# Kernel tuning notes

Hardware: AMD Instinct MI355X
Metric: run time of the kernel (lower is better)

## Reference

```python
import jax, jax.numpy as jnp
import numpy as np

E, D, A, EMB, V = 2048, 512, 512, 512, 10000
B, HW, L = 64, 14, 52
P = HW * HW  # num_pixels
T = L - 1    # max decode length (we force max caption length == L)


def setup_inputs() -> dict:
    key = jax.random.key(0)
    ks = jax.random.split(key, 24)
    s = 0.02
    inp = {
        "encoder_out": jax.random.normal(ks[0], (B, HW, HW, E), jnp.float32),
        "encoded_captions": jax.random.randint(ks[1], (B, L), 0, V),
        "caption_lengths": jax.random.randint(ks[2], (B, 1), 2, L + 1).at[0, 0].set(L),
        # attention
        "W_ea": jax.random.normal(ks[3], (A, E)) * s, "b_ea": jnp.zeros((A,)),
        "W_da": jax.random.normal(ks[4], (A, D)) * s, "b_da": jnp.zeros((A,)),
        "w_fa": jax.random.normal(ks[5], (1, A)) * s, "b_fa": jnp.zeros((1,)),
        # embedding (uniform(-0.1,0.1) as in init_weights)
        "emb_table": jax.random.uniform(ks[6], (V, EMB), minval=-0.1, maxval=0.1),
        # LSTMCell: gates order i,f,g,o
        "W_ih": jax.random.normal(ks[7], (4 * D, EMB + E)) * s, "b_ih": jnp.zeros((4 * D,)),
        "W_hh": jax.random.normal(ks[8], (4 * D, D)) * s, "b_hh": jnp.zeros((4 * D,)),
        "W_init_h": jax.random.normal(ks[9], (D, E)) * s, "b_init_h": jnp.zeros((D,)),
        "W_init_c": jax.random.normal(ks[10], (D, E)) * s, "b_init_c": jnp.zeros((D,)),
        "W_fb": jax.random.normal(ks[11], (E, D)) * s, "b_fb": jnp.zeros((E,)),
        "W_fc": jax.random.uniform(ks[12], (V, D), minval=-0.1, maxval=0.1), "b_fc": jnp.zeros((V,)),
    }
    return inp


def _decode(encoder_out, encoded_captions, caption_lengths,
            W_ea, b_ea, W_da, b_da, w_fa, b_fa, emb_table,
            W_ih, b_ih, W_hh, b_hh, W_init_h, b_init_h,
            W_init_c, b_init_c, W_fb, b_fb, W_fc, b_fc):
    enc = encoder_out.reshape(B, -1, E)  # (B,P,E)
    lengths = caption_lengths[:, 0]
    order = jnp.argsort(-lengths)  # descending, stable
    lengths = lengths[order]
    enc = enc[order]
    caps = encoded_captions[order]
    dec_len = lengths - 1  # (B,)

    embeds = emb_table[caps]  # (B,L,EMB)
    mean_enc = enc.mean(axis=1)  # (B,E)
    h0 = mean_enc @ W_init_h.T + b_init_h
    c0 = mean_enc @ W_init_c.T + b_init_c

    # encoder side of attention is time-invariant; compute once
    att1 = jnp.einsum('bpe,ae->bpa', enc, W_ea) + b_ea  # (B,P,A)

    emb_seq = jnp.transpose(embeds[:, :T, :], (1, 0, 2))  # (T,B,EMB)
    ts = jnp.arange(T)

    def step(carry, xs):
        h, c = carry
        t, emb_t = xs
        mask = (t < dec_len)  # (B,)
        mf = mask[:, None].astype(h.dtype)
        # Bahdanau attention
        att2 = h @ W_da.T + b_da  # (B,A)
        e = jnp.einsum('bpa,a->bp', jax.nn.relu(att1 + att2[:, None, :]), w_fa[0]) + b_fa[0]
        alpha = jax.nn.softmax(e, axis=1)  # (B,P)
        awe = jnp.einsum('bpe,bp->be', enc, alpha)
        gate = jax.nn.sigmoid(h @ W_fb.T + b_fb)
        awe = gate * awe
        # LSTMCell
        x = jnp.concatenate([emb_t, awe], axis=1)  # (B, EMB+E)
        gates = x @ W_ih.T + b_ih + h @ W_hh.T + b_hh
        i_, f_, g_, o_ = jnp.split(gates, 4, axis=1)
        c2 = jax.nn.sigmoid(f_) * c + jax.nn.sigmoid(i_) * jnp.tanh(g_)
        h2 = jax.nn.sigmoid(o_) * jnp.tanh(c2)
        preds = h2 @ W_fc.T + b_fc  # dropout is identity in eval/reference
        h = jnp.where(mask[:, None], h2, h)
        c = jnp.where(mask[:, None], c2, c)
        return (h, c), (preds * mf, alpha * mf)

    (_, _), (preds_seq, alpha_seq) = jax.lax.scan(step, (h0, c0), (ts, emb_seq))
    predictions = jnp.transpose(preds_seq, (1, 0, 2))  # (B,T,V)
    alphas = jnp.transpose(alpha_seq, (1, 0, 2))       # (B,T,P)
    return predictions, caps, dec_len, alphas, order


def reference(encoder_out, encoded_captions, caption_lengths,
              W_ea, b_ea, W_da, b_da, w_fa, b_fa, emb_table,
              W_ih, b_ih, W_hh, b_hh, W_init_h, b_init_h,
              W_init_c, b_init_c, W_fb, b_fb, W_fc, b_fc):
    return _decode(encoder_out, encoded_captions, caption_lengths,
                   W_ea, b_ea, W_da, b_da, w_fa, b_fa, emb_table,
                   W_ih, b_ih, W_hh, b_hh, W_init_h, b_init_h,
                   W_init_c, b_init_c, W_fb, b_fb, W_fc, b_fc)
```

## Files before the change

### kernel.cpp

```cpp
#include <hip/hip_runtime.h>
#include <cmath>

#define NB 64
#define NP 196
#define NE 2048
#define NV 10000
#define NL 52
#define NT 51

typedef unsigned short bf16_t;
typedef __attribute__((ext_vector_type(8))) short bf16x8;
typedef __attribute__((ext_vector_type(4))) float f32x4;

__device__ inline unsigned short f2bf(float f){
  unsigned int x = __float_as_uint(f);
  unsigned int r = x + 0x7fffu + ((x>>16)&1u);
  return (unsigned short)(r>>16);
}
__device__ inline float bf2f(unsigned short u){ return __uint_as_float(((unsigned int)u)<<16); }
__device__ inline float sigm(float x){ return 1.f/(1.f+expf(-x)); }

__global__ void k_sort(const int* __restrict__ cap_len, const int* __restrict__ caps,
                       int* __restrict__ order, int* __restrict__ dlen, int* __restrict__ caps_s,
                       int* __restrict__ nact,
                       float* __restrict__ out_caps, float* __restrict__ out_dlen, float* __restrict__ out_order){
  __shared__ int len_s[NB];
  __shared__ int ord_s[NB];
  __shared__ int dls[NB];
  int t = threadIdx.x;
  len_s[t] = cap_len[t];
  __syncthreads();
  int li = len_s[t]; int rank = 0;
  for(int j=0;j<NB;j++){ int lj = len_s[j]; rank += ((lj > li) || (lj==li && j<t)) ? 1 : 0; }
  ord_s[rank] = t;
  __syncthreads();
  int ob = ord_s[t];
  order[t] = ob; out_order[t] = (float)ob;
  int ls = len_s[ob]; dlen[t] = ls-1; out_dlen[t] = (float)(ls-1); dls[t] = ls-1;
  for(int l=0;l<NL;l++){ int cv = caps[ob*NL + l]; caps_s[t*NL+l]=cv; out_caps[t*NL+l] = (float)cv; }
  __syncthreads();
  if(t < NT){
    int cnt=0;
    for(int b=0;b<NB;b++) cnt += (dls[b] > t) ? 1 : 0;
    nact[t] = cnt;
  }
}

__global__ __launch_bounds__(256) void k_cvt4(const float* __restrict__ src, bf16_t* __restrict__ dst, int n4){
  int i = blockIdx.x*blockDim.x + threadIdx.x;
  int stride = gridDim.x*blockDim.x;
  for(; i<n4; i+=stride){
    float4 v = ((const float4*)src)[i];
    unsigned long long p = (unsigned long long)f2bf(v.x)
        | ((unsigned long long)f2bf(v.y)<<16)
        | ((unsigned long long)f2bf(v.z)<<32)
        | ((unsigned long long)f2bf(v.w)<<48);
    ((unsigned long long*)dst)[i] = p;
  }
}

__global__ __launch_bounds__(256) void k_cvt2d4(const float* __restrict__ src, int rows, int cols,
                                                bf16_t* __restrict__ dst, int dld, int doff){
  int n4 = rows*cols/4;
  int c4n = cols/4;
  int i = blockIdx.x*blockDim.x + threadIdx.x;
  int stride = gridDim.x*blockDim.x;
  for(; i<n4; i+=stride){
    int r = i / c4n, c4 = i % c4n;
    float4 v = ((const float4*)src)[i];
    unsigned long long p = (unsigned long long)f2bf(v.x)
        | ((unsigned long long)f2bf(v.y)<<16)
        | ((unsigned long long)f2bf(v.z)<<32)
        | ((unsigned long long)f2bf(v.w)<<48);
    *(unsigned long long*)(dst + (size_t)r*dld + doff + c4*4) = p;
  }
}

__global__ __launch_bounds__(256) void k_mean(const float* __restrict__ enc, const int* __restrict__ order,
                                              bf16_t* __restrict__ me_s){
  int bs = blockIdx.x; int ec = blockIdx.y; int e = ec*256 + threadIdx.x;
  int ob = order[bs];
  const float* p = enc + (size_t)ob*NP*NE + e;
  float acc=0.f;
  for(int q=0;q<NP;q++) acc += p[(size_t)q*NE];
  me_s[(size_t)bs*NE + e] = f2bf(acc * (1.0f/NP));
}

__global__ __launch_bounds__(256) void k_emb(const int* __restrict__ caps_s, const float* __restrict__ emb_table,
                                             bf16_t* __restrict__ embAll){
  int b = blockIdx.x, t = blockIdx.y, tid = threadIdx.x;
  int cap = caps_s[b*NL + t];
  bf16_t* dst = embAll + ((size_t)t*NB + b)*512;
  const float* src = emb_table + (size_t)cap*512;
  dst[tid]       = f2bf(src[tid]);
  dst[tid + 256] = f2bf(src[tid + 256]);
}

template<int MODE>
__global__ __launch_bounds__(256) void k_big(const bf16_t* __restrict__ A, int lda, int Kdim,
      const bf16_t* __restrict__ Bw, int nrowsB,
      const float* __restrict__ bias, float* __restrict__ outf, bf16_t* __restrict__ outb,
      const int* __restrict__ dlen){
  __shared__ __align__(16) char smem_raw[36864];
  bf16_t (*As)[72] = (bf16_t(*)[72])smem_raw;
  bf16_t (*Bs)[72] = (bf16_t(*)[72])(smem_raw + 18432);
  int nblk = blockIdx.x, mblk = blockIdx.y;
  int tid = threadIdx.x;
  int w = tid>>6, l = tid&63;
  int moff = (w>>1)*64, noff = (w&1)*64;
  f32x4 acc[4][4] = {};
  const int mbase = mblk*128, nbase = nblk*128;
  for(int k0=0; k0<Kdim; k0+=64){
    __syncthreads();
    for(int u=0;u<4;u++){
      int lin = u*256 + tid; int row = lin>>3; int col = (lin&7)*8;
      *(bf16x8*)(&As[row][col]) = *(const bf16x8*)(A + (size_t)(mbase+row)*lda + k0 + col);
      int rB = nbase+row; if(MODE==2 && rB >= nrowsB) rB = nrowsB-1;
      *(bf16x8*)(&Bs[row][col]) = *(const bf16x8*)(Bw + (size_t)rB*lda + k0 + col);
    }
    __syncthreads();
    for(int kk=0;kk<2;kk++){
      bf16x8 af[4], bfr[4];
      for(int m=0;m<4;m++) af[m] = *(bf16x8*)(&As[moff + 16*m + (l&15)][kk*32 + (l>>4)*8]);
      for(int n=0;n<4;n++) bfr[n] = *(bf16x8*)(&Bs[noff + 16*n + (l&15)][kk*32 + (l>>4)*8]);
      for(int m=0;m<4;m++)
        for(int n=0;n<4;n++)
          acc[m][n] = __builtin_amdgcn_mfma_f32_16x16x32_bf16(af[m], bfr[n], acc[m][n], 0,0,0);
    }
  }
  if(MODE==0){
    for(int m=0;m<4;m++) for(int n=0;n<4;n++){
      int col = nbase + noff + 16*n + (l&15);
      float bi = bias[col];
      for(int r=0;r<4;r++){
        int row = mbase + moff + 16*m + (l>>4)*4 + r;
        outb[(size_t)row*512 + col] = f2bf(acc[m][n][r] + bi);
      }
    }
  } else {
    float* st = (float*)smem_raw;
    for(int h=0; h<2; ++h){
      __syncthreads();
      if((w>>1)==h){
        for(int m=0;m<4;m++) for(int n=0;n<4;n++)
          for(int r=0;r<4;r++)
            st[(16*m + (l>>4)*4 + r)*128 + noff + 16*n + (l&15)] = acc[m][n][r];
      }
      __syncthreads();
      for(int rr = tid>>5; rr<64; rr+=8){
        int row = mbase + h*64 + rr;
        if(row < NT*NB){
          int tt = row>>6, bb = row&63;
          int cc = (tid&31)*4;
          int col0 = nbase + cc;
          if(col0 < NV){
            float4 v = *(float4*)&st[rr*128 + cc];
            float4 bi4 = *(const float4*)&bias[col0];
            v.x+=bi4.x; v.y+=bi4.y; v.z+=bi4.z; v.w+=bi4.w;
            if(tt >= dlen[bb]){ v.x=0.f; v.y=0.f; v.z=0.f; v.w=0.f; }
            *(float4*)&outf[((size_t)bb*NT + tt)*NV + col0] = v;
          }
        }
      }
    }
  }
}

template<int KSL>
__global__ __launch_bounds__(256) void k_gemm_part(const bf16_t* __restrict__ Ax, int lda,
        const bf16_t* __restrict__ W, int ldw, float* __restrict__ part, int N){
  __shared__ bf16_t As[64][KSL+8];
  int ntile = blockIdx.x, ks = blockIdx.y;
  int tid = threadIdx.x; int w = tid>>6, l = tid&63;
  int k0 = ks*KSL;
  constexpr int UPR = KSL/8;
  constexpr int UPT = 64*UPR/256;
  for(int u=0;u<UPT;u++){
    int lin = u*256 + tid; int row = lin/UPR; int col = (lin%UPR)*8;
    *(bf16x8*)(&As[row][col]) = *(const bf16x8*)(Ax + (size_t)row*lda + k0 + col);
  }
  __syncthreads();
  f32x4 acc[4][4] = {};
  int nbase = ntile*256 + w*64;
  for(int kk=0; kk<KSL/32; kk++){
    bf16x8 af[4], bfr[4];
    for(int m=0;m<4;m++) af[m] = *(bf16x8*)(&As[16*m + (l&15)][kk*32 + (l>>4)*8]);
    for(int n=0;n<4;n++) bfr[n] = *(const bf16x8*)(W + (size_t)(nbase + 16*n + (l&15))*ldw + k0 + kk*32 + (l>>4)*8);
    for(int m=0;m<4;m++)
      for(int n=0;n<4;n++)
        acc[m][n] = __builtin_amdgcn_mfma_f32_16x16x32_bf16(af[m], bfr[n], acc[m][n], 0,0,0);
  }
  float* po = part + (size_t)ks*64*N;
  for(int m=0;m<4;m++) for(int n=0;n<4;n++){
    int col = nbase + 16*n + (l&15);
    for(int r=0;r<4;r++){
      int row = 16*m + (l>>4)*4 + r;
      po[(size_t)row*N + col] = acc[m][n][r];
    }
  }
}

__global__ __launch_bounds__(256) void k_init_fin(const float* __restrict__ part,
        const float* __restrict__ b_ih_, const float* __restrict__ b_ic_,
        float* __restrict__ c, bf16_t* __restrict__ h0){
  int idx = blockIdx.x*256 + threadIdx.x;
  int b_ = idx>>9, d = idx&511;
  float h = b_ih_[d], cc = b_ic_[d];
  for(int ks=0;ks<4;ks++){
    const float* p = part + (size_t)ks*64*1024 + (size_t)b_*1024;
    h += p[d]; cc += p[512+d];
  }
  c[idx] = cc;
  h0[(size_t)b_*512 + d] = f2bf(h);
}

__global__ __launch_bounds__(256) void k_e(const bf16_t* __restrict__ att1,
    const float* __restrict__ a2g, const float* __restrict__ b_da,
    const float* __restrict__ w_fa, const float* __restrict__ b_fa,
    const int* __restrict__ order, const int* __restrict__ nact,
    float* __restrict__ e_out, int t){
  int b_ = blockIdx.x, pg = blockIdx.y, tid = threadIdx.x;
  if(b_ >= nact[t]) return;
  int w = tid>>6, l = tid&63;
  int ob = order[b_];
  const float* pa0 = a2g + ((size_t)0*NB + b_)*2560;
  const float* pa1 = a2g + ((size_t)1*NB + b_)*2560;
  const float* pa2 = a2g + ((size_t)2*NB + b_)*2560;
  const float* pa3 = a2g + ((size_t)3*NB + b_)*2560;
  float ar[8], wr[8];
  #pragma unroll
  for(int q=0;q<8;q++){
    int i = l*8 + q;
    ar[q] = pa0[i] + pa1[i] + pa2[i] + pa3[i] + b_da[i];
    wr[q] = w_fa[i];
  }
  float bfa0 = b_fa[0];
  for(int pl=w; pl<49; pl+=4){
    int p = pg*49 + pl;
    bf16x8 a1v = *(const bf16x8*)(att1 + ((size_t)ob*NP + p)*512 + l*8);
    float s = 0.f;
    #pragma unroll
    for(int q=0;q<8;q++){
      float v = bf2f((unsigned short)a1v[q]) + ar[q];
      v = v>0.f ? v : 0.f;
      s += v*wr[q];
    }
    #pragma unroll
    for(int off=32;off;off>>=1) s += __shfl_down(s, off);
    if(l==0) e_out[b_*NP + p] = s + bfa0;
  }
}

__global__ __launch_bounds__(256) void k_awe(const bf16_t* __restrict__ enc, const float* __restrict__ e_in,
    const float* __restrict__ a2g, const float* __restrict__ b_fb,
    const int* __restrict__ order, const int* __restrict__ nact,
    float* __restrict__ alphas_out, bf16_t* __restrict__ xh_awe, int t){
  int b_ = blockIdx.x, y = blockIdx.y, tid = threadIdx.x;
  if(b_ >= nact[t]){
    if(y==0 && tid<NP) alphas_out[((size_t)b_*NT + t)*NP + tid] = 0.f;
    return;
  }
  __shared__ float al[200];
  __shared__ float red[8];
  __shared__ float aw[4][512];
  int w = tid>>6, l = tid&63;
  float v = (tid<NP)? e_in[b_*NP + tid] : -1e30f;
  float m = v;
  #pragma unroll
  for(int off=32;off;off>>=1) m = fmaxf(m, __shfl_down(m, off));
  if(l==0) red[w] = m;
  __syncthreads();
  float mx = fmaxf(fmaxf(red[0],red[1]), fmaxf(red[2],red[3]));
  float ex = (tid<NP)? expf(v - mx) : 0.f;
  float s2 = ex;
  #pragma unroll
  for(int off=32;off;off>>=1) s2 += __shfl_down(s2, off);
  if(l==0) red[4+w] = s2;
  __syncthreads();
  float inv = 1.f/(red[4]+red[5]+red[6]+red[7]);
  if(tid<NP){
    float a = ex*inv;
    al[tid] = a;
    if(y==0) alphas_out[((size_t)b_*NT + t)*NP + tid] = a;
  }
  __syncthreads();
  int ob = order[b_];
  int j0 = y*512 + l*8;
  float a8[8] = {};
  const bf16_t* ep = enc + (size_t)ob*NP*NE + j0;
  int p0 = w*49;
  #pragma unroll 4
  for(int pp=0; pp<49; ++pp){
    int p = p0 + pp;
    bf16x8 ev = *(const bf16x8*)(ep + (size_t)p*NE);
    float alp = al[p];
    #pragma unroll
    for(int q=0;q<8;q++) a8[q] += alp*bf2f((unsigned short)ev[q]);
  }
  #pragma unroll
  for(int q=0;q<8;q++) aw[w][l*8 + q] = a8[q];
  __syncthreads();
  const float* pa0 = a2g + ((size_t)0*NB + b_)*2560;
  const float* pa1 = a2g + ((size_t)1*NB + b_)*2560;
  const float* pa2 = a2g + ((size_t)2*NB + b_)*2560;
  const float* pa3 = a2g + ((size_t)3*NB + b_)*2560;
  int jl = tid*2;
  int j  = y*512 + jl;
  #pragma unroll
  for(int q=0;q<2;q++){
    float s = aw[0][jl+q] + aw[1][jl+q] + aw[2][jl+q] + aw[3][jl+q];
    int jj = 512 + j + q;
    float gpre = pa0[jj] + pa1[jj] + pa2[jj] + pa3[jj] + b_fb[j + q];
    xh_awe[(size_t)b_*2048 + j + q] = f2bf(sigm(gpre)*s);
  }
}

__global__ __launch_bounds__(256) void k_gatecell(const bf16_t* __restrict__ embT,
    const bf16_t* __restrict__ xh_awe, const bf16_t* __restrict__ hr,
    bf16_t* __restrict__ hw, const bf16_t* __restrict__ Wcat,
    const float* __restrict__ b_ih, const float* __restrict__ b_hh,
    float* __restrict__ cbuf, bf16_t* __restrict__ h2all,
    const int* __restrict__ dlen, int t){
  __shared__ float part[4][64][16];
  int j = blockIdx.x, tid = threadIdx.x;
  int w = tid>>6, l = tid&63;
  int n_ = l&15;
  int wrow = (n_>>2)*512 + j*4 + (n_&3);
  const bf16_t* wp = Wcat + (size_t)wrow*3072;
  f32x4 acc[4] = {};
  int k0w = w*768;
  for(int kk=0;kk<24;kk++){
    int col = k0w + kk*32 + (l>>4)*8;
    bf16x8 af[4], bg;
    if(col < 512){
      #pragma unroll
      for(int m=0;m<4;m++) af[m] = *(const bf16x8*)(embT + (size_t)(16*m + n_)*512 + col);
    } else if(col < 2560){
      #pragma unroll
      for(int m=0;m<4;m++) af[m] = *(const bf16x8*)(xh_awe + (size_t)(16*m + n_)*2048 + col - 512);
    } else {
      #pragma unroll
      for(int m=0;m<4;m++) af[m] = *(const bf16x8*)(hr + (size_t)(16*m + n_)*512 + col - 2560);
    }
    bg = *(const bf16x8*)(wp + col);
    #pragma unroll
    for(int m=0;m<4;m++)
      acc[m] = __builtin_amdgcn_mfma_f32_16x16x32_bf16(af[m], bg, acc[m], 0,0,0);
  }
  #pragma unroll
  for(int m=0;m<4;m++)
    #pragma unroll
    for(int r=0;r<4;r++)
      part[w][16*m + (l>>4)*4 + r][n_] = acc[m][r];
  __syncthreads();
  int b = tid>>2, c = tid&3;
  int dg = j*4 + c;
  float gs[4];
  #pragma unroll
  for(int g=0;g<4;g++){
    gs[g] = b_ih[g*512+dg] + b_hh[g*512+dg]
          + part[0][b][g*4+c] + part[1][b][g*4+c]
          + part[2][b][g*4+c] + part[3][b][g*4+c];
  }
  float oldc = cbuf[b*512 + dg];
  float c2 = sigm(gs[1])*oldc + sigm(gs[0])*tanhf(gs[2]);
  float h2 = sigm(gs[3])*tanhf(c2);
  bool mk = t < dlen[b];
  if(mk) cbuf[b*512 + dg] = c2;
  hw[(size_t)b*512 + dg] = mk ? f2bf(h2) : hr[(size_t)b*512 + dg];
  h2all[((size_t)t*NB + b)*512 + dg] = f2bf(h2);
}

extern "C" void kernel_launch(void* const* d_in, const int* in_sizes, int n_in,
                              void* d_out, int out_size, void* d_ws, size_t ws_size,
                              hipStream_t stream){
  (void)in_sizes; (void)n_in; (void)out_size; (void)ws_size;
  const float* encoder_out      = (const float*)d_in[0];
  const int*   encoded_captions = (const int*)d_in[1];
  const int*   caption_lengths  = (const int*)d_in[2];
  const float* W_ea = (const float*)d_in[3];  const float* b_ea = (const float*)d_in[4];
  const float* W_da = (const float*)d_in[5];  const float* b_da = (const float*)d_in[6];
  const float* w_fa = (const float*)d_in[7];  const float* b_fa = (const float*)d_in[8];
  const float* emb_table = (const float*)d_in[9];
  const float* W_ih = (const float*)d_in[10]; const float* b_ih = (const float*)d_in[11];
  const float* W_hh = (const float*)d_in[12]; const float* b_hh = (const float*)d_in[13];
  const float* W_init_h = (const float*)d_in[14]; const float* b_init_h = (const float*)d_in[15];
  const float* W_init_c = (const float*)d_in[16]; const float* b_init_c = (const float*)d_in[17];
  const float* W_fb = (const float*)d_in[18]; const float* b_fb = (const float*)d_in[19];
  const float* W_fc = (const float*)d_in[20]; const float* b_fc = (const float*)d_in[21];

  float* out_preds = (float*)d_out;
  float* out_caps  = out_preds + (size_t)NB*NT*NV;
  float* out_dlen  = out_caps + NB*NL;
  float* out_alph  = out_dlen + NB;
  float* out_order = out_alph + (size_t)NB*NT*NP;

  char* ws = (char*)d_ws;
  size_t off = 0;
  auto alloc = [&](size_t bytes)->size_t{ size_t r = off; off += (bytes + 255) & ~(size_t)255; return r; };
  bf16_t* enc_b   = (bf16_t*)(ws + alloc((size_t)12544*2048*2));
  char*   reg_att1 = ws + alloc((size_t)12544*512*2);
  bf16_t* att1_b  = (bf16_t*)reg_att1;
  float*  ipart   = (float*)reg_att1;
  char*   reg_h2   = ws + alloc((size_t)3328*512*2);
  bf16_t* h2all_b = (bf16_t*)reg_h2;
  bf16_t* Wea_b   = (bf16_t*)reg_h2;
  bf16_t* Wdafb_b = (bf16_t*)(ws + alloc((size_t)2560*512*2));
  bf16_t* Wcat_b  = (bf16_t*)(ws + alloc((size_t)2048*3072*2));
  bf16_t* Wfc_b   = (bf16_t*)(ws + alloc((size_t)10000*512*2));
  char*   reg_wi  = ws + alloc((size_t)1024*2048*2);
  bf16_t* Winit_b = (bf16_t*)reg_wi;
  bf16_t* embAll  = (bf16_t*)reg_wi;
  bf16_t* me_b    = (bf16_t*)(ws + alloc((size_t)64*2048*2));
  bf16_t* xh_awe  = (bf16_t*)(ws + alloc((size_t)64*2048*2));
  bf16_t* hbuf0   = (bf16_t*)(ws + alloc((size_t)64*512*2));
  bf16_t* hbuf1   = (bf16_t*)(ws + alloc((size_t)64*512*2));
  float*  c_f     = (float*)(ws + alloc((size_t)64*512*4));
  float*  a2gp_f  = (float*)(ws + alloc((size_t)4*64*2560*4));
  float*  e_f     = (float*)(ws + alloc((size_t)64*196*4));
  int*    order_i = (int*)(ws + alloc(64*4));
  int*    dlen_i  = (int*)(ws + alloc(64*4));
  int*    nact_i  = (int*)(ws + alloc(64*4));
  int*    caps_i  = (int*)(ws + alloc((size_t)64*52*4));

  k_sort<<<1,64,0,stream>>>(caption_lengths, encoded_captions, order_i, dlen_i, caps_i, nact_i,
                            out_caps, out_dlen, out_order);
  k_cvt4<<<2048,256,0,stream>>>(encoder_out, enc_b, 12544*2048/4);
  k_cvt4<<<512,256,0,stream>>>(W_ea, Wea_b, 512*2048/4);
  k_cvt4<<<256,256,0,stream>>>(W_da, Wdafb_b, 512*512/4);
  k_cvt4<<<512,256,0,stream>>>(W_fb, Wdafb_b + 512*512, 2048*512/4);
  k_cvt2d4<<<1024,256,0,stream>>>(W_ih, 2048, 2560, Wcat_b, 3072, 0);
  k_cvt2d4<<<512,256,0,stream>>>(W_hh, 2048, 512, Wcat_b, 3072, 2560);
  k_cvt4<<<512,256,0,stream>>>(W_init_h, Winit_b, 512*2048/4);
  k_cvt4<<<512,256,0,stream>>>(W_init_c, Winit_b + 512*2048, 512*2048/4);
  k_cvt4<<<1024,256,0,stream>>>(W_fc, Wfc_b, 10000*512/4);
  k_mean<<<dim3(64,8),256,0,stream>>>(encoder_out, order_i, me_b);
  k_gemm_part<512><<<dim3(4,4),256,0,stream>>>(me_b, 2048, Winit_b, 2048, ipart, 1024);
  k_init_fin<<<128,256,0,stream>>>(ipart, b_init_h, b_init_c, c_f, hbuf0);
  k_emb<<<dim3(NB,NT),256,0,stream>>>(caps_i, emb_table, embAll);
  k_big<0><<<dim3(4,98),256,0,stream>>>(enc_b, 2048, 2048, Wea_b, 512, b_ea, nullptr, att1_b, nullptr);
  k_gemm_part<128><<<dim3(10,4),256,0,stream>>>(hbuf0, 512, Wdafb_b, 512, a2gp_f, 2560);

  bf16_t* hb[2] = { hbuf0, hbuf1 };
  for(int t=0;t<NT;t++){
    bf16_t* hr = hb[t&1];
    bf16_t* hw = hb[(t&1)^1];
    k_e<<<dim3(64,4),256,0,stream>>>(att1_b, a2gp_f, b_da, w_fa, b_fa, order_i, nact_i, e_f, t);
    k_awe<<<dim3(64,4),256,0,stream>>>(enc_b, e_f, a2gp_f, b_fb, order_i, nact_i,
                                       out_alph, xh_awe, t);
    k_gatecell<<<128,256,0,stream>>>(embAll + (size_t)t*NB*512, xh_awe, hr, hw, Wcat_b,
                                     b_ih, b_hh, c_f, h2all_b, dlen_i, t);
    k_gemm_part<128><<<dim3(10,4),256,0,stream>>>(hw, 512, Wdafb_b, 512, a2gp_f, 2560);
  }
  k_big<2><<<dim3(79,26),256,0,stream>>>(h2all_b, 512, 512, Wfc_b, NV, b_fc, out_preds, nullptr, dlen_i);
}
```

Measured before the change: 2.696 ms.

## Fuse decoder-attention GEMV into energy kernel and remap big GEMM blocks per XCD

```diff
diff --git a/kernel.cpp b/kernel.cpp
--- a/kernel.cpp
+++ b/kernel.cpp
@@ -76,13 +76,13 @@
   }
 }
 
-__global__ __launch_bounds__(256) void k_mean(const float* __restrict__ enc, const int* __restrict__ order,
+__global__ __launch_bounds__(256) void k_mean(const bf16_t* __restrict__ encb, const int* __restrict__ order,
                                               bf16_t* __restrict__ me_s){
   int bs = blockIdx.x; int ec = blockIdx.y; int e = ec*256 + threadIdx.x;
   int ob = order[bs];
-  const float* p = enc + (size_t)ob*NP*NE + e;
+  const bf16_t* p = encb + (size_t)ob*NP*NE + e;
   float acc=0.f;
-  for(int q=0;q<NP;q++) acc += p[(size_t)q*NE];
+  for(int q=0;q<NP;q++) acc += bf2f(p[(size_t)q*NE]);
   me_s[(size_t)bs*NE + e] = f2bf(acc * (1.0f/NP));
 }
 
@@ -104,7 +104,16 @@
   __shared__ __align__(16) char smem_raw[36864];
   bf16_t (*As)[72] = (bf16_t(*)[72])smem_raw;
   bf16_t (*Bs)[72] = (bf16_t(*)[72])(smem_raw + 18432);
-  int nblk = blockIdx.x, mblk = blockIdx.y;
+  int lid = blockIdx.x;
+  int nblk, mblk;
+  if(MODE==0){
+    int wg = (lid&7)*49 + (lid>>3);
+    mblk = wg>>2; nblk = wg&3;
+  } else {
+    int xcd = lid&7; int idx = lid>>3;
+    int wg = (xcd<6) ? xcd*257 + idx : 1542 + (xcd-6)*256 + idx;
+    nblk = wg/26; mblk = wg - nblk*26;
+  }
   int tid = threadIdx.x;
   int w = tid>>6, l = tid&63;
   int moff = (w>>1)*64, noff = (w&1)*64;
@@ -214,27 +223,61 @@
   h0[(size_t)b_*512 + d] = f2bf(h);
 }
 
-__global__ __launch_bounds__(256) void k_e(const bf16_t* __restrict__ att1,
-    const float* __restrict__ a2g, const float* __restrict__ b_da,
+__global__ __launch_bounds__(256) void k_ea(const bf16_t* __restrict__ att1,
+    const bf16_t* __restrict__ hr, const bf16_t* __restrict__ Wdafb,
+    const float* __restrict__ b_da, const float* __restrict__ b_fb,
     const float* __restrict__ w_fa, const float* __restrict__ b_fa,
     const int* __restrict__ order, const int* __restrict__ nact,
-    float* __restrict__ e_out, int t){
+    float* __restrict__ e_out, float* __restrict__ gpre_out, int t){
   int b_ = blockIdx.x, pg = blockIdx.y, tid = threadIdx.x;
   if(b_ >= nact[t]) return;
+  __shared__ float hs[512];
+  __shared__ float att2s[512];
   int w = tid>>6, l = tid&63;
+  unsigned int hv = *(const unsigned int*)(hr + (size_t)b_*512 + tid*2);
+  hs[tid*2]   = __uint_as_float(hv<<16);
+  hs[tid*2+1] = __uint_as_float(hv & 0xffff0000u);
+  __syncthreads();
+  {
+    int n0 = tid*2;
+    const bf16_t* w0 = Wdafb + (size_t)n0*512;
+    float a0=0.f, a1=0.f;
+    for(int k=0;k<512;k+=8){
+      bf16x8 va = *(const bf16x8*)(w0 + k);
+      bf16x8 vb = *(const bf16x8*)(w0 + 512 + k);
+      #pragma unroll
+      for(int q=0;q<8;q++){
+        float hq = hs[k+q];
+        a0 += hq*bf2f((unsigned short)va[q]);
+        a1 += hq*bf2f((unsigned short)vb[q]);
+      }
+    }
+    att2s[n0]   = a0 + b_da[n0];
+    att2s[n0+1] = a1 + b_da[n0+1];
+  }
+  {
+    int j0 = pg*512 + tid*2;
+    const bf16_t* w0 = Wdafb + (size_t)(512 + j0)*512;
+    float g0=0.f, g1=0.f;
+    for(int k=0;k<512;k+=8){
+      bf16x8 va = *(const bf16x8*)(w0 + k);
+      bf16x8 vb = *(const bf16x8*)(w0 + 512 + k);
+      #pragma unroll
+      for(int q=0;q<8;q++){
+        float hq = hs[k+q];
+        g0 += hq*bf2f((unsigned short)va[q]);
+        g1 += hq*bf2f((unsigned short)vb[q]);
+      }
+    }
+    gpre_out[(size_t)b_*2048 + j0]   = g0 + b_fb[j0];
+    gpre_out[(size_t)b_*2048 + j0+1] = g1 + b_fb[j0+1];
+  }
+  __syncthreads();
+  float ar[8], wr[8];
+  #pragma unroll
+  for(int q=0;q<8;q++){ ar[q] = att2s[l*8+q]; wr[q] = w_fa[l*8+q]; }
+  float bfa0 = b_fa[0];
   int ob = order[b_];
-  const float* pa0 = a2g + ((size_t)0*NB + b_)*2560;
-  const float* pa1 = a2g + ((size_t)1*NB + b_)*2560;
-  const float* pa2 = a2g + ((size_t)2*NB + b_)*2560;
-  const float* pa3 = a2g + ((size_t)3*NB + b_)*2560;
-  float ar[8], wr[8];
-  #pragma unroll
-  for(int q=0;q<8;q++){
-    int i = l*8 + q;
-    ar[q] = pa0[i] + pa1[i] + pa2[i] + pa3[i] + b_da[i];
-    wr[q] = w_fa[i];
-  }
-  float bfa0 = b_fa[0];
   for(int pl=w; pl<49; pl+=4){
     int p = pg*49 + pl;
     bf16x8 a1v = *(const bf16x8*)(att1 + ((size_t)ob*NP + p)*512 + l*8);
@@ -251,8 +294,8 @@
   }
 }
 
-__global__ __launch_bounds__(256) void k_awe(const bf16_t* __restrict__ enc, const float* __restrict__ e_in,
-    const float* __restrict__ a2g, const float* __restrict__ b_fb,
+__global__ __launch_bounds__(256) void k_aweg(const bf16_t* __restrict__ enc, const float* __restrict__ e_in,
+    const float* __restrict__ gpre,
     const int* __restrict__ order, const int* __restrict__ nact,
     float* __restrict__ alphas_out, bf16_t* __restrict__ xh_awe, int t){
   int b_ = blockIdx.x, y = blockIdx.y, tid = threadIdx.x;
@@ -300,18 +343,13 @@
   #pragma unroll
   for(int q=0;q<8;q++) aw[w][l*8 + q] = a8[q];
   __syncthreads();
-  const float* pa0 = a2g + ((size_t)0*NB + b_)*2560;
-  const float* pa1 = a2g + ((size_t)1*NB + b_)*2560;
-  const float* pa2 = a2g + ((size_t)2*NB + b_)*2560;
-  const float* pa3 = a2g + ((size_t)3*NB + b_)*2560;
   int jl = tid*2;
   int j  = y*512 + jl;
   #pragma unroll
   for(int q=0;q<2;q++){
     float s = aw[0][jl+q] + aw[1][jl+q] + aw[2][jl+q] + aw[3][jl+q];
-    int jj = 512 + j + q;
-    float gpre = pa0[jj] + pa1[jj] + pa2[jj] + pa3[jj] + b_fb[j + q];
-    xh_awe[(size_t)b_*2048 + j + q] = f2bf(sigm(gpre)*s);
+    float gp = gpre[(size_t)b_*2048 + j + q];
+    xh_awe[(size_t)b_*2048 + j + q] = f2bf(sigm(gp)*s);
   }
 }
 
@@ -416,7 +454,7 @@
   bf16_t* hbuf0   = (bf16_t*)(ws + alloc((size_t)64*512*2));
   bf16_t* hbuf1   = (bf16_t*)(ws + alloc((size_t)64*512*2));
   float*  c_f     = (float*)(ws + alloc((size_t)64*512*4));
-  float*  a2gp_f  = (float*)(ws + alloc((size_t)4*64*2560*4));
+  float*  gpre_f  = (float*)(ws + alloc((size_t)64*2048*4));
   float*  e_f     = (float*)(ws + alloc((size_t)64*196*4));
   int*    order_i = (int*)(ws + alloc(64*4));
   int*    dlen_i  = (int*)(ws + alloc(64*4));
@@ -434,23 +472,22 @@
   k_cvt4<<<512,256,0,stream>>>(W_init_h, Winit_b, 512*2048/4);
   k_cvt4<<<512,256,0,stream>>>(W_init_c, Winit_b + 512*2048, 512*2048/4);
   k_cvt4<<<1024,256,0,stream>>>(W_fc, Wfc_b, 10000*512/4);
-  k_mean<<<dim3(64,8),256,0,stream>>>(encoder_out, order_i, me_b);
+  k_mean<<<dim3(64,8),256,0,stream>>>(enc_b, order_i, me_b);
   k_gemm_part<512><<<dim3(4,4),256,0,stream>>>(me_b, 2048, Winit_b, 2048, ipart, 1024);
   k_init_fin<<<128,256,0,stream>>>(ipart, b_init_h, b_init_c, c_f, hbuf0);
   k_emb<<<dim3(NB,NT),256,0,stream>>>(caps_i, emb_table, embAll);
-  k_big<0><<<dim3(4,98),256,0,stream>>>(enc_b, 2048, 2048, Wea_b, 512, b_ea, nullptr, att1_b, nullptr);
-  k_gemm_part<128><<<dim3(10,4),256,0,stream>>>(hbuf0, 512, Wdafb_b, 512, a2gp_f, 2560);
+  k_big<0><<<392,256,0,stream>>>(enc_b, 2048, 2048, Wea_b, 512, b_ea, nullptr, att1_b, nullptr);
 
   bf16_t* hb[2] = { hbuf0, hbuf1 };
   for(int t=0;t<NT;t++){
     bf16_t* hr = hb[t&1];
     bf16_t* hw = hb[(t&1)^1];
-    k_e<<<dim3(64,4),256,0,stream>>>(att1_b, a2gp_f, b_da, w_fa, b_fa, order_i, nact_i, e_f, t);
-    k_awe<<<dim3(64,4),256,0,stream>>>(enc_b, e_f, a2gp_f, b_fb, order_i, nact_i,
-                                       out_alph, xh_awe, t);
+    k_ea<<<dim3(64,4),256,0,stream>>>(att1_b, hr, Wdafb_b, b_da, b_fb, w_fa, b_fa,
+                                      order_i, nact_i, e_f, gpre_f, t);
+    k_aweg<<<dim3(64,4),256,0,stream>>>(enc_b, e_f, gpre_f, order_i, nact_i,
+                                        out_alph, xh_awe, t);
     k_gatecell<<<128,256,0,stream>>>(embAll + (size_t)t*NB*512, xh_awe, hr, hw, Wcat_b,
                                      b_ih, b_hh, c_f, h2all_b, dlen_i, t);
-    k_gemm_part<128><<<dim3(10,4),256,0,stream>>>(hw, 512, Wdafb_b, 512, a2gp_f, 2560);
-  }
-  k_big<2><<<dim3(79,26),256,0,stream>>>(h2all_b, 512, 512, Wfc_b, NV, b_fc, out_preds, nullptr, dlen_i);
-}
+  }
+  k_big<2><<<2054,256,0,stream>>>(h2all_b, 512, 512, Wfc_b, NV, b_fc, out_preds, nullptr, dlen_i);
+}
```

After: 4.139 ms. 53.5% more time.
